# Kernel optimization log

Hardware: AMD Instinct MI355X
Metric: run time of the kernel (lower is better)

## Reference

```python
import jax, jax.numpy as jnp
import numpy as np

D_MODEL = 1024
NUM_HEADS = 16
D_LATENT = 256
HEAD_DIM = D_MODEL // NUM_HEADS
BATCH = 2048
SEQ = 32


def setup_inputs() -> dict:
    key = jax.random.key(0)
    ks = jax.random.split(key, 9)
    s = 1.0 / np.sqrt(D_MODEL)
    sl = 1.0 / np.sqrt(D_LATENT)
    return {
        "x": jax.random.normal(ks[0], (BATCH, SEQ, D_MODEL), dtype=jnp.float32),
        "memory": jax.random.normal(ks[1], (BATCH, SEQ, D_LATENT), dtype=jnp.float32),
        "W_q": jax.random.normal(ks[2], (D_MODEL, D_MODEL), dtype=jnp.float32) * s,
        "W_k": jax.random.normal(ks[3], (D_MODEL, D_MODEL), dtype=jnp.float32) * s,
        "W_v": jax.random.normal(ks[4], (D_MODEL, D_MODEL), dtype=jnp.float32) * s,
        "W_o": jax.random.normal(ks[5], (D_MODEL, D_MODEL), dtype=jnp.float32) * s,
        "W_down_kv": jax.random.normal(ks[6], (D_MODEL, D_LATENT), dtype=jnp.float32) * s,
        "W_up_k": jax.random.normal(ks[7], (D_LATENT, D_MODEL), dtype=jnp.float32) * sl,
        "W_up_v": jax.random.normal(ks[8], (D_LATENT, D_MODEL), dtype=jnp.float32) * sl,
    }


def reference(x, memory, W_q, W_k, W_v, W_o, W_down_kv, W_up_k, W_up_v):
    B, S, _ = x.shape
    q = x @ W_q                     # [B,S,D]
    k = x @ W_k
    v = x @ W_v
    latent_kv = (k + v) @ W_down_kv  # [B,S,L]
    latent_kv = jnp.nan_to_num((latent_kv + memory) * 0.5)
    k_rec = latent_kv @ W_up_k       # [B,S,D]
    v_rec = latent_kv @ W_up_v
    # split heads: [B,H,S,hd]
    qh = q.reshape(B, S, NUM_HEADS, HEAD_DIM).transpose(0, 2, 1, 3)
    kh = k_rec.reshape(B, S, NUM_HEADS, HEAD_DIM).transpose(0, 2, 1, 3)
    vh = v_rec.reshape(B, S, NUM_HEADS, HEAD_DIM).transpose(0, 2, 1, 3)
    # NOTE: faithful to source — scale is sqrt(d_model), not sqrt(head_dim)
    scores = jnp.einsum("bhqd,bhkd->bhqk", qh, kh) / jnp.sqrt(jnp.float32(D_MODEL))
    scores = jnp.nan_to_num(scores, nan=0.0, posinf=10.0, neginf=-10.0)
    attn = jax.nn.softmax(scores, axis=-1)
    ctx = jnp.einsum("bhqk,bhkd->bhqd", attn, vh)
    ctx = ctx.transpose(0, 2, 1, 3).reshape(B, S, D_MODEL)
    out = ctx @ W_o
    return out, latent_kv
```

## Files before the change

### kernel.cpp

```cpp
#include <hip/hip_runtime.h>
#include <hip/hip_bf16.h>

typedef unsigned short u16;
typedef unsigned int u32;
typedef __attribute__((ext_vector_type(8))) __bf16 bf16x8;
typedef __attribute__((ext_vector_type(8))) unsigned short u16x8;
typedef __attribute__((ext_vector_type(4))) float floatx4;
typedef __attribute__((ext_vector_type(16))) float floatx16;

#define AS1 __attribute__((address_space(1)))
#define AS3 __attribute__((address_space(3)))

__device__ __forceinline__ u16 f2bf(float f) {
  unsigned u = __float_as_uint(f);
  u += 0x7fffu + ((u >> 16) & 1u);
  return (u16)(u >> 16);
}

__device__ __forceinline__ void g2lds16(const u16* g, u16* l) {
  __builtin_amdgcn_global_load_lds((AS1 void*)g, (AS3 void*)l, 16, 0, 0);
}

__global__ __launch_bounds__(256) void k_cvt_bf16(const float* __restrict__ s,
                                                  u16* __restrict__ d, long n) {
  long i = ((long)blockIdx.x * blockDim.x + threadIdx.x) * 8;
  long stride = (long)gridDim.x * blockDim.x * 8;
  for (; i < n; i += stride) {
    float4 a = *(const float4*)(s + i);
    float4 b = *(const float4*)(s + i + 4);
    u16x8 o;
    o[0] = f2bf(a.x); o[1] = f2bf(a.y); o[2] = f2bf(a.z); o[3] = f2bf(a.w);
    o[4] = f2bf(b.x); o[5] = f2bf(b.y); o[6] = f2bf(b.z); o[7] = f2bf(b.w);
    *(u16x8*)(d + i) = o;
  }
}

__global__ __launch_bounds__(256) void k_addcvt(const float* __restrict__ s0,
                                                const float* __restrict__ s1,
                                                u16* __restrict__ d, long n) {
  long i = ((long)blockIdx.x * blockDim.x + threadIdx.x) * 8;
  long stride = (long)gridDim.x * blockDim.x * 8;
  for (; i < n; i += stride) {
    float4 a0 = *(const float4*)(s0 + i);
    float4 a1 = *(const float4*)(s0 + i + 4);
    float4 b0 = *(const float4*)(s1 + i);
    float4 b1 = *(const float4*)(s1 + i + 4);
    u16x8 o;
    o[0] = f2bf(a0.x + b0.x); o[1] = f2bf(a0.y + b0.y);
    o[2] = f2bf(a0.z + b0.z); o[3] = f2bf(a0.w + b0.w);
    o[4] = f2bf(a1.x + b1.x); o[5] = f2bf(a1.y + b1.y);
    o[6] = f2bf(a1.z + b1.z); o[7] = f2bf(a1.w + b1.w);
    *(u16x8*)(d + i) = o;
  }
}

__global__ __launch_bounds__(256) void k_tcvt(const float* __restrict__ s,
                                              u16* __restrict__ d, int R, int C) {
  __shared__ float t[32][33];
  const int lx = threadIdx.x, ly = threadIdx.y;
  const int bx = blockIdx.x * 32;
  const int by = blockIdx.y * 32;
  #pragma unroll
  for (int i = 0; i < 32; i += 8)
    t[ly + i][lx] = s[(size_t)(by + ly + i) * C + bx + lx];
  __syncthreads();
  #pragma unroll
  for (int i = 0; i < 32; i += 8)
    d[(size_t)(bx + ly + i) * R + by + lx] = f2bf(t[lx][ly + i]);
}

#define MFMA16(a, b, c) c = __builtin_amdgcn_mfma_f32_16x16x32_bf16(a, b, c, 0, 0, 0)
#define MFMA32(a, b, c) c = __builtin_amdgcn_mfma_f32_32x32x16_bf16(a, b, c, 0, 0, 0)

template <int MODE>
__global__ __launch_bounds__(256, 3) void gemm128(
    const u16* __restrict__ A, const u16* __restrict__ Bt,
    int M, int N, int K, int ntn,
    u16* __restrict__ Cb, float* __restrict__ Cf,
    const float* __restrict__ memp, float* __restrict__ latf, u16* __restrict__ latb) {
  __shared__ u16 As[128 * 64];
  __shared__ u16 Bs[128 * 64];
  const int tid = threadIdx.x;
  const int lane = tid & 63;
  const int wid = tid >> 6;
  const int wr = wid >> 1, wc = wid & 1;

  int bid = blockIdx.x;
  {
    const int nwg = gridDim.x;
    const int q = nwg >> 3, r = nwg & 7;
    const int xcd = bid & 7, idx = bid >> 3;
    bid = (xcd < r ? xcd * (q + 1) : r * (q + 1) + (xcd - r) * q) + idx;
  }
  const int mt = bid / ntn, nt = bid % ntn;
  const int m0 = mt * 128, n0 = nt * 128;

  const int fr = lane & 15;
  const int g8 = (lane >> 4) * 8;
  const int xr = (lane & 7) * 8;

  floatx4 acc[4][4];
  #pragma unroll
  for (int i = 0; i < 4; i++)
    #pragma unroll
    for (int j = 0; j < 4; j++) acc[i][j] = 0.0f;

  const u16* Ag0 = A + (size_t)m0 * K;
  const u16* Bg0 = Bt + (size_t)n0 * K;

  for (int kt = 0; kt < K; kt += 64) {
    #pragma unroll
    for (int p = 0; p < 4; p++) {
      int ci = p * 256 + tid;
      int row = ci >> 3;
      int kc = ((ci & 7) ^ (row & 7)) * 8;
      g2lds16(Ag0 + (size_t)row * K + kt + kc, &As[ci * 8]);
    }
    #pragma unroll
    for (int p = 0; p < 4; p++) {
      int ci = p * 256 + tid;
      int row = ci >> 3;
      int kc = ((ci & 7) ^ (row & 7)) * 8;
      g2lds16(Bg0 + (size_t)row * K + kt + kc, &Bs[ci * 8]);
    }
    __syncthreads();
    #pragma unroll
    for (int kk = 0; kk < 64; kk += 32) {
      const int koff = kk + g8;
      bf16x8 af[4], bfv[4];
      #pragma unroll
      for (int i = 0; i < 4; i++)
        af[i] = *(const bf16x8*)&As[(wr * 64 + i * 16 + fr) * 64 + (koff ^ xr)];
      #pragma unroll
      for (int j = 0; j < 4; j++)
        bfv[j] = *(const bf16x8*)&Bs[(wc * 64 + j * 16 + fr) * 64 + (koff ^ xr)];
      #pragma unroll
      for (int i = 0; i < 4; i++)
        #pragma unroll
        for (int j = 0; j < 4; j++)
          MFMA16(af[i], bfv[j], acc[i][j]);
    }
    __syncthreads();
  }

  #pragma unroll
  for (int i = 0; i < 4; i++) {
    const int mb = m0 + wr * 64 + i * 16 + ((lane >> 4) * 4);
    #pragma unroll
    for (int j = 0; j < 4; j++) {
      const int cb = n0 + wc * 64 + j * 16 + (lane & 15);
      #pragma unroll
      for (int r = 0; r < 4; r++) {
        const int m = mb + r;
        const float v = acc[i][j][r];
        if (MODE == 0) {
          Cb[(size_t)m * N + cb] = f2bf(v);
        } else if (MODE == 1) {
          if (n0 < 1024) {
            Cb[(size_t)m * 1024 + cb] = f2bf(v);
          } else {
            int lc = cb - 1024;
            float lv = (v + memp[(size_t)m * 256 + lc]) * 0.5f;
            latf[(size_t)m * 256 + lc] = lv;
            latb[(size_t)m * 256 + lc] = f2bf(lv);
          }
        } else {
          Cf[(size_t)m * N + cb] = v;
        }
      }
    }
  }
}

__device__ __forceinline__ void pack_lds(u16* T, const floatx16& d,
                                         int col, int hi, bf16x8& f0, bf16x8& f1) {
  #pragma unroll
  for (int i = 0; i < 8; i++) {
    const int r = 2 * i;
    const int rr = (r & 3) + 8 * (r >> 2) + 4 * hi;
    const u32 wv = (u32)f2bf(d[r]) | ((u32)f2bf(d[r + 1]) << 16);
    *(u32*)&T[col * 40 + rr] = wv;
  }
  f0 = *(const bf16x8*)&T[col * 40 + hi * 8];
  f1 = *(const bf16x8*)&T[col * 40 + 16 + hi * 8];
}

__global__ __launch_bounds__(256, 3) void k_attn2(
    const u16* __restrict__ Lb,
    u16* __restrict__ Q,
    const u16* __restrict__ Wuk,
    const u16* __restrict__ WuvT)
{
  __shared__ u16 Ls[32][264];
  __shared__ u16 LsT[256][40];
  __shared__ u16 Tw[4][32][40];
  const int tid = threadIdx.x;
  const long tok0 = (long)blockIdx.x * 32;

  {
    const int key = tid >> 3, c0 = (tid & 7) * 32;
    #pragma unroll
    for (int u = 0; u < 4; u++) {
      u16x8 v = *(const u16x8*)(Lb + (tok0 + key) * 256 + c0 + u * 8);
      *(u16x8*)&Ls[key][c0 + u * 8] = v;
      #pragma unroll
      for (int j = 0; j < 8; j++) LsT[c0 + u * 8 + j][key] = v[j];
    }
  }
  __syncthreads();

  const int w = tid >> 6;
  const int lane = tid & 63;
  const int col = lane & 31;
  const int hi = lane >> 5;
  const int hi8 = hi * 8;
  const int rhi4 = hi * 4;
  u16* T = &Tw[w][0][0];

  #pragma unroll 1
  for (int hh = 0; hh < 4; hh++) {
    const int h = w + hh * 4;

    const u16* qbase = Q + (tok0 + col) * 1024 + h * 64 + hi8;
    bf16x8 qf[4];
    #pragma unroll
    for (int ks = 0; ks < 4; ks++)
      qf[ks] = *(const bf16x8*)(qbase + ks * 16);

    floatx16 St;
    #pragma unroll
    for (int r = 0; r < 16; r++) St[r] = 0.0f;
    #pragma unroll
    for (int mi = 0; mi < 8; mi++) {
      floatx16 qt;
      #pragma unroll
      for (int r = 0; r < 16; r++) qt[r] = 0.0f;
      #pragma unroll
      for (int ks = 0; ks < 4; ks++) {
        bf16x8 af = *(const bf16x8*)(Wuk + (size_t)(mi * 32 + col) * 1024 +
                                     h * 64 + ks * 16 + hi8);
        MFMA32(af, qf[ks], qt);
      }
      bf16x8 qg0, qg1;
      pack_lds(T, qt, col, hi, qg0, qg1);
      bf16x8 la0 = *(const bf16x8*)&Ls[col][mi * 32 + hi8];
      MFMA32(la0, qg0, St);
      bf16x8 la1 = *(const bf16x8*)&Ls[col][mi * 32 + 16 + hi8];
      MFMA32(la1, qg1, St);
    }

    float p[16];
    float mx = -3.4e38f;
    #pragma unroll
    for (int r = 0; r < 16; r++) { p[r] = St[r] * 0.03125f; mx = fmaxf(mx, p[r]); }
    mx = fmaxf(mx, __shfl_xor(mx, 32, 64));
    float sm = 0.0f;
    #pragma unroll
    for (int r = 0; r < 16; r++) { p[r] = __expf(p[r] - mx); sm += p[r]; }
    sm += __shfl_xor(sm, 32, 64);
    const float rs = 1.0f / sm;
    floatx16 Pt;
    #pragma unroll
    for (int r = 0; r < 16; r++) Pt[r] = p[r] * rs;
    bf16x8 pg0, pg1;
    pack_lds(T, Pt, col, hi, pg0, pg1);

    floatx16 cacc0, cacc1;
    #pragma unroll
    for (int r = 0; r < 16; r++) { cacc0[r] = 0.0f; cacc1[r] = 0.0f; }
    const u16* wv0 = WuvT + (size_t)(h * 64 + col) * 256;
    const u16* wv1 = WuvT + (size_t)(h * 64 + 32 + col) * 256;
    #pragma unroll
    for (int mi = 0; mi < 8; mi++) {
      floatx16 ct;
      #pragma unroll
      for (int r = 0; r < 16; r++) ct[r] = 0.0f;
      bf16x8 lt0 = *(const bf16x8*)&LsT[mi * 32 + col][hi8];
      MFMA32(lt0, pg0, ct);
      bf16x8 lt1 = *(const bf16x8*)&LsT[mi * 32 + col][16 + hi8];
      MFMA32(lt1, pg1, ct);
      bf16x8 cg0, cg1;
      pack_lds(T, ct, col, hi, cg0, cg1);
      #pragma unroll
      for (int ksl = 0; ksl < 2; ksl++) {
        bf16x8 cg = ksl ? cg1 : cg0;
        bf16x8 b0 = *(const bf16x8*)(wv0 + mi * 32 + ksl * 16 + hi8);
        bf16x8 b1 = *(const bf16x8*)(wv1 + mi * 32 + ksl * 16 + hi8);
        MFMA32(cg, b0, cacc0);
        MFMA32(cg, b1, cacc1);
      }
    }

    #pragma unroll
    for (int r = 0; r < 16; r++) {
      const int rr = (r & 3) + 8 * (r >> 2) + rhi4;
      u16* orow = Q + (tok0 + rr) * 1024 + h * 64;
      orow[col] = f2bf(cacc0[r]);
      orow[32 + col] = f2bf(cacc1[r]);
    }
  }
}

extern "C" void kernel_launch(void* const* d_in, const int* in_sizes, int n_in,
                              void* d_out, int out_size, void* d_ws, size_t ws_size,
                              hipStream_t stream) {
  const float* x    = (const float*)d_in[0];
  const float* mem  = (const float*)d_in[1];
  const float* W_q  = (const float*)d_in[2];
  const float* W_k  = (const float*)d_in[3];
  const float* W_v  = (const float*)d_in[4];
  const float* W_o  = (const float*)d_in[5];
  const float* W_dn = (const float*)d_in[6];
  const float* W_uk = (const float*)d_in[7];
  const float* W_uv = (const float*)d_in[8];
  float* out  = (float*)d_out;
  float* latf = out + (size_t)67108864;

  char* wp = (char*)d_ws;
  u16* Qb   = (u16*)wp; wp += (size_t)65536 * 1024 * 2;
  u16* Lb   = (u16*)wp; wp += (size_t)65536 * 256 * 2;
  u16* WAt  = (u16*)wp; wp += (size_t)1280 * 1024 * 2;
  u16* WuvT = (u16*)wp; wp += (size_t)1024 * 256 * 2;
  u16* Wot  = (u16*)wp; wp += (size_t)1024 * 1024 * 2;
  u16* Wdt  = (u16*)wp; wp += (size_t)256 * 1024 * 2;
  u16* Wkv  = (u16*)wp; wp += (size_t)1024 * 1024 * 2;
  u16* Wukb = (u16*)wp; wp += (size_t)256 * 1024 * 2;

  u16* Xb = (u16*)d_out;

  dim3 b256(256);
  dim3 tb(32, 8);
  k_cvt_bf16<<<4096, b256, 0, stream>>>(x, Xb, (long)67108864);
  k_addcvt<<<512, b256, 0, stream>>>(W_k, W_v, Wkv, (long)1048576);
  k_cvt_bf16<<<128, b256, 0, stream>>>(W_uk, Wukb, (long)262144);
  k_tcvt<<<dim3(32, 32), tb, 0, stream>>>(W_q, WAt, 1024, 1024);
  k_tcvt<<<dim3(8, 32),  tb, 0, stream>>>(W_dn, Wdt, 1024, 256);
  k_tcvt<<<dim3(32, 8),  tb, 0, stream>>>(W_uv, WuvT, 256, 1024);
  k_tcvt<<<dim3(32, 32), tb, 0, stream>>>(W_o, Wot, 1024, 1024);

  gemm128<0><<<16, b256, 0, stream>>>(
      Wdt, Wkv, 256, 1024, 1024, 8, WAt + (size_t)1024 * 1024,
      nullptr, nullptr, nullptr, nullptr);

  gemm128<1><<<5120, b256, 0, stream>>>(
      Xb, WAt, 65536, 1280, 1024, 10, Qb, nullptr, mem, latf, Lb);

  k_attn2<<<2048, b256, 0, stream>>>(Lb, Qb, Wukb, WuvT);

  gemm128<2><<<4096, b256, 0, stream>>>(
      Qb, Wot, 65536, 1024, 1024, 8, nullptr, out, nullptr, nullptr, nullptr);
}
```

Baseline: 898.1 us.

## Replace LDS transpose scratch with cross-lane shuffles and double attention block width

The MFMA output-to-operand relayout in the attention kernel now uses __shfl_xor across wave halves instead of writing to and reading back from a per-wave LDS scratch tile. The per-wave scratch buffer is removed. The block size grows from 256 to 512 threads, so each wave processes 2 heads instead of 4 and the latent tile staging is spread over more threads. This is meant to cut LDS traffic and barrier-free scratch round trips and to raise parallelism per block. In exchange it adds shuffle instructions and register pressure under the new launch bounds.

```diff
diff --git a/kernel.cpp b/kernel.cpp
--- a/kernel.cpp
+++ b/kernel.cpp
@@ -5,6 +5,7 @@
 typedef unsigned int u32;
 typedef __attribute__((ext_vector_type(8))) __bf16 bf16x8;
 typedef __attribute__((ext_vector_type(8))) unsigned short u16x8;
+typedef __attribute__((ext_vector_type(4))) unsigned int u32x4;
 typedef __attribute__((ext_vector_type(4))) float floatx4;
 typedef __attribute__((ext_vector_type(16))) float floatx16;
 
@@ -172,20 +173,24 @@
   }
 }
 
-__device__ __forceinline__ void pack_lds(u16* T, const floatx16& d,
-                                         int col, int hi, bf16x8& f0, bf16x8& f1) {
-  #pragma unroll
-  for (int i = 0; i < 8; i++) {
-    const int r = 2 * i;
-    const int rr = (r & 3) + 8 * (r >> 2) + 4 * hi;
-    const u32 wv = (u32)f2bf(d[r]) | ((u32)f2bf(d[r + 1]) << 16);
-    *(u32*)&T[col * 40 + rr] = wv;
-  }
-  f0 = *(const bf16x8*)&T[col * 40 + hi * 8];
-  f1 = *(const bf16x8*)&T[col * 40 + 16 + hi * 8];
-}
-
-__global__ __launch_bounds__(256, 3) void k_attn2(
+__device__ __forceinline__ void pack_shfl(const floatx16& d, int hi,
+                                          bf16x8& f0, bf16x8& f1) {
+  u32 c[8];
+  #pragma unroll
+  for (int i = 0; i < 8; i++)
+    c[i] = (u32)f2bf(d[2 * i]) | ((u32)f2bf(d[2 * i + 1]) << 16);
+  u32 p0 = __shfl_xor(c[0], 32, 64), p1 = __shfl_xor(c[1], 32, 64);
+  u32 p2 = __shfl_xor(c[2], 32, 64), p3 = __shfl_xor(c[3], 32, 64);
+  u32 p4 = __shfl_xor(c[4], 32, 64), p5 = __shfl_xor(c[5], 32, 64);
+  u32 p6 = __shfl_xor(c[6], 32, 64), p7 = __shfl_xor(c[7], 32, 64);
+  u32x4 w0, w1;
+  if (hi) { w0 = u32x4{p2, p3, c[2], c[3]}; w1 = u32x4{p6, p7, c[6], c[7]}; }
+  else    { w0 = u32x4{c[0], c[1], p0, p1}; w1 = u32x4{c[4], c[5], p4, p5}; }
+  f0 = __builtin_bit_cast(bf16x8, w0);
+  f1 = __builtin_bit_cast(bf16x8, w1);
+}
+
+__global__ __launch_bounds__(512, 4) void k_attn2(
     const u16* __restrict__ Lb,
     u16* __restrict__ Q,
     const u16* __restrict__ Wuk,
@@ -193,14 +198,13 @@
 {
   __shared__ u16 Ls[32][264];
   __shared__ u16 LsT[256][40];
-  __shared__ u16 Tw[4][32][40];
   const int tid = threadIdx.x;
   const long tok0 = (long)blockIdx.x * 32;
 
   {
-    const int key = tid >> 3, c0 = (tid & 7) * 32;
-    #pragma unroll
-    for (int u = 0; u < 4; u++) {
+    const int key = tid >> 4, c0 = (tid & 15) * 16;
+    #pragma unroll
+    for (int u = 0; u < 2; u++) {
       u16x8 v = *(const u16x8*)(Lb + (tok0 + key) * 256 + c0 + u * 8);
       *(u16x8*)&Ls[key][c0 + u * 8] = v;
       #pragma unroll
@@ -215,11 +219,10 @@
   const int hi = lane >> 5;
   const int hi8 = hi * 8;
   const int rhi4 = hi * 4;
-  u16* T = &Tw[w][0][0];
 
   #pragma unroll 1
-  for (int hh = 0; hh < 4; hh++) {
-    const int h = w + hh * 4;
+  for (int hh = 0; hh < 2; hh++) {
+    const int h = w + hh * 8;
 
     const u16* qbase = Q + (tok0 + col) * 1024 + h * 64 + hi8;
     bf16x8 qf[4];
@@ -242,7 +245,7 @@
         MFMA32(af, qf[ks], qt);
       }
       bf16x8 qg0, qg1;
-      pack_lds(T, qt, col, hi, qg0, qg1);
+      pack_shfl(qt, hi, qg0, qg1);
       bf16x8 la0 = *(const bf16x8*)&Ls[col][mi * 32 + hi8];
       MFMA32(la0, qg0, St);
       bf16x8 la1 = *(const bf16x8*)&Ls[col][mi * 32 + 16 + hi8];
@@ -263,7 +266,7 @@
     #pragma unroll
     for (int r = 0; r < 16; r++) Pt[r] = p[r] * rs;
     bf16x8 pg0, pg1;
-    pack_lds(T, Pt, col, hi, pg0, pg1);
+    pack_shfl(Pt, hi, pg0, pg1);
 
     floatx16 cacc0, cacc1;
     #pragma unroll
@@ -280,7 +283,7 @@
       bf16x8 lt1 = *(const bf16x8*)&LsT[mi * 32 + col][16 + hi8];
       MFMA32(lt1, pg1, ct);
       bf16x8 cg0, cg1;
-      pack_lds(T, ct, col, hi, cg0, cg1);
+      pack_shfl(ct, hi, cg0, cg1);
       #pragma unroll
       for (int ksl = 0; ksl < 2; ksl++) {
         bf16x8 cg = ksl ? cg1 : cg0;
@@ -345,7 +348,7 @@
   gemm128<1><<<5120, b256, 0, stream>>>(
       Xb, WAt, 65536, 1280, 1024, 10, Qb, nullptr, mem, latf, Lb);
 
-  k_attn2<<<2048, b256, 0, stream>>>(Lb, Qb, Wukb, WuvT);
+  k_attn2<<<2048, dim3(512), 0, stream>>>(Lb, Qb, Wukb, WuvT);
 
   gemm128<2><<<4096, b256, 0, stream>>>(
       Qb, Wot, 65536, 1024, 1024, 8, nullptr, out, nullptr, nullptr, nullptr);
```

New measurement: 1.026 ms. 1.14x slower.
